# Optimization experiments

Measured on AMD Instinct MI355X. Metric: run time of the kernel, lower is better.

The kernel has to match this reference:

```python
import jax, jax.numpy as jnp
import numpy as np

N_WAY = 5
K_SHOT = 5
GAMMA = 20.0    # self.gamma
GAMMA2 = 10.0   # self.gamma2
ALPHA = 0.5     # self.katz_factor
EPS = 1e-16


def setup_inputs() -> dict:
    key = jax.random.key(0)
    k1, k2 = jax.random.split(key)
    feat = jax.random.normal(k1, (2 * N_WAY * K_SHOT, 640, 14, 14), dtype=jnp.float32)
    query_y = jax.random.randint(k2, (N_WAY * K_SHOT,), 0, N_WAY, dtype=jnp.int64)
    return {"feat": feat, "query_y": query_y}


def _predicts(feat):
    n_support = N_WAY * K_SHOT
    query = feat[n_support:]                      # (q, c, h, w)
    # adaptive_max_pool2d(query, w) with h == w is the identity, so the
    # (buggy-but-literal) torch code uses the query tensor as "support".
    support = query
    q, c, h, w = query.shape
    hw = h * w
    # class prototypes: mean over shots -> (n_way, c, hw)
    sup = support.reshape(N_WAY, K_SHOT, c, hw).mean(axis=1)
    qry = query.reshape(q, c, hw)
    # cosine metric: l2-normalize along channel axis
    sup = sup / (EPS + jnp.linalg.norm(sup, axis=1, keepdims=True))
    qry = qry / (EPS + jnp.linalg.norm(qry, axis=1, keepdims=True))
    # S[n, m_q, s, m_s] = <qry[n,:,m_q], sup[s,:,m_s]> ; then fold class dim into M_s
    S = jnp.einsum('qcm,scn->qmsn', qry, sup).reshape(q, hw, N_WAY * hw)
    N, M_q, M_s = S.shape
    # row-stochastic transition matrices (exp/max/sum == softmax of gamma*S)
    T_sq = jax.nn.softmax(GAMMA * S, axis=-1)                              # (N, M_q, M_s)
    T_qs = jax.nn.softmax(GAMMA2 * jnp.swapaxes(S, -1, -2), axis=-1)       # (N, M_s, M_q)
    # bipartite block matrix T = [[0, T_sq^T], [T_qs^T, 0]]
    top = jnp.concatenate([jnp.zeros((N, M_s, M_s), S.dtype),
                           jnp.swapaxes(T_sq, -1, -2)], axis=-1)
    bot = jnp.concatenate([jnp.swapaxes(T_qs, -1, -2),
                           jnp.zeros((N, M_q, M_q), S.dtype)], axis=-1)
    T = jnp.concatenate([top, bot], axis=-2)                               # (N, M_s+M_q, M_s+M_q)
    eye = jnp.eye(M_s + M_q, dtype=S.dtype)
    ones = jnp.ones((N, M_s + M_q, 1), S.dtype)
    # (inv(I - a T) - I) @ 1  ==  solve(I - a T, 1) - 1 (same math, no explicit inverse)
    katz = jnp.linalg.solve(eye[None] - ALPHA * T, ones)[..., 0] - 1.0     # (N, M_s+M_q)
    partial = katz[:, :M_s]
    partial = partial / partial.sum(axis=-1, keepdims=True)
    predicts = partial.reshape(N, N_WAY, -1).sum(axis=-1)                  # (N, n_way)
    return predicts


def reference(feat, query_y):
    return _predicts(feat)
```

## Files before the change

### kernel.cpp

```cpp
#include <hip/hip_runtime.h>
#include <math.h>

#define NQ     25
#define NWAY   5
#define KSHOT  5
#define CC     640
#define HW     196
#define NSL    980
#define NSLP   992
#define RPQ    208
#define BROWS  1024
#define MST    200
#define MRA    208
#define GAMMA  20.0f
#define GAMMA2 10.0f
#define NITER  8

typedef __bf16 bf16;
typedef _Float16 f16;
typedef __attribute__((ext_vector_type(8))) __bf16 bf16x8;
typedef __attribute__((ext_vector_type(4))) float f32x4;

__global__ __launch_bounds__(256) void k_norm(const float* __restrict__ feat,
                                              bf16* __restrict__ qnbt,
                                              bf16* __restrict__ snbt) {
    const int by = blockIdx.y;
    const int lx = threadIdx.x & 15;
    const int cg = threadIdx.x >> 4;
    const int l  = blockIdx.x * 16 + lx;
    const bool act = (l < HW);
    const int c0 = cg * 40;
    __shared__ float pr[16][17];

    float xv[40];
    float ss = 0.f;
    if (by < NQ) {
        const float* f = feat + (size_t)(NQ + by) * CC * HW;
#pragma unroll
        for (int i = 0; i < 40; ++i) {
            float x = act ? f[(c0 + i) * HW + l] : 0.f;
            xv[i] = x; ss += x * x;
        }
    } else {
        const int s = by - NQ;
        const float* f = feat + (size_t)(NQ + s * KSHOT) * CC * HW;
        const size_t img = (size_t)CC * HW;
#pragma unroll
        for (int i = 0; i < 40; ++i) {
            float m = 0.f;
            if (act) {
                const float* p = f + (c0 + i) * HW + l;
                m = 0.2f * (p[0] + p[img] + p[2 * img] + p[3 * img] + p[4 * img]);
            }
            xv[i] = m; ss += m * m;
        }
    }
    pr[cg][lx] = ss;
    __syncthreads();
    if (cg == 0) {
        float a = 0.f;
#pragma unroll
        for (int k = 0; k < 16; ++k) a += pr[k][lx];
        pr[0][lx] = 1.f / (1e-16f + sqrtf(a));
    }
    __syncthreads();
    const float inv = pr[0][lx];
    if (act) {
        bf16* o = (by < NQ) ? (qnbt + ((size_t)by * RPQ + l) * CC)
                            : (snbt + ((size_t)(by - NQ) * HW + l) * CC);
#pragma unroll
        for (int i = 0; i < 40; ++i) o[c0 + i] = (bf16)(xv[i] * inv);
    }
}

#define ASTR2 72
__global__ __launch_bounds__(256) void k_sgemm(const bf16* __restrict__ qnbt,
                                               const bf16* __restrict__ snbt,
                                               f16* __restrict__ S) {
    const int q  = blockIdx.z;
    const int m0 = blockIdx.y * 80;
    const int n0 = blockIdx.x * 128;
    __shared__ bf16 As[128 * ASTR2];
    __shared__ bf16 Bs[128 * ASTR2];
    const int t = threadIdx.x;
    const int lane = t & 63, w = t >> 6;
    const int wr = w >> 1, wc = w & 1;
    const int lo = lane & 15, hi = lane >> 4;
    const int sr = t >> 1, sh = (t & 1) * 32;

    const bf16* Aq = qnbt + (size_t)q * RPQ * CC;
    f32x4 acc[4][4] = {};

    for (int k0 = 0; k0 < CC; k0 += 64) {
        bf16x8 a0 = *reinterpret_cast<const bf16x8*>(&Aq[(size_t)(m0 + sr) * CC + k0 + sh]);
        bf16x8 a1 = *reinterpret_cast<const bf16x8*>(&Aq[(size_t)(m0 + sr) * CC + k0 + sh + 8]);
        bf16x8 a2 = *reinterpret_cast<const bf16x8*>(&Aq[(size_t)(m0 + sr) * CC + k0 + sh + 16]);
        bf16x8 a3 = *reinterpret_cast<const bf16x8*>(&Aq[(size_t)(m0 + sr) * CC + k0 + sh + 24]);
        bf16x8 b0 = *reinterpret_cast<const bf16x8*>(&snbt[(size_t)(n0 + sr) * CC + k0 + sh]);
        bf16x8 b1 = *reinterpret_cast<const bf16x8*>(&snbt[(size_t)(n0 + sr) * CC + k0 + sh + 8]);
        bf16x8 b2 = *reinterpret_cast<const bf16x8*>(&snbt[(size_t)(n0 + sr) * CC + k0 + sh + 16]);
        bf16x8 b3 = *reinterpret_cast<const bf16x8*>(&snbt[(size_t)(n0 + sr) * CC + k0 + sh + 24]);
        __syncthreads();
        *reinterpret_cast<bf16x8*>(&As[sr * ASTR2 + sh])      = a0;
        *reinterpret_cast<bf16x8*>(&As[sr * ASTR2 + sh + 8])  = a1;
        *reinterpret_cast<bf16x8*>(&As[sr * ASTR2 + sh + 16]) = a2;
        *reinterpret_cast<bf16x8*>(&As[sr * ASTR2 + sh + 24]) = a3;
        *reinterpret_cast<bf16x8*>(&Bs[sr * ASTR2 + sh])      = b0;
        *reinterpret_cast<bf16x8*>(&Bs[sr * ASTR2 + sh + 8])  = b1;
        *reinterpret_cast<bf16x8*>(&Bs[sr * ASTR2 + sh + 16]) = b2;
        *reinterpret_cast<bf16x8*>(&Bs[sr * ASTR2 + sh + 24]) = b3;
        __syncthreads();
#pragma unroll
        for (int kk = 0; kk < 2; ++kk) {
            bf16x8 af[4], bf[4];
#pragma unroll
            for (int mi = 0; mi < 4; ++mi)
                af[mi] = *reinterpret_cast<const bf16x8*>(
                    &As[(wr * 64 + mi * 16 + lo) * ASTR2 + kk * 32 + hi * 8]);
#pragma unroll
            for (int ni = 0; ni < 4; ++ni)
                bf[ni] = *reinterpret_cast<const bf16x8*>(
                    &Bs[(wc * 64 + ni * 16 + lo) * ASTR2 + kk * 32 + hi * 8]);
#pragma unroll
            for (int mi = 0; mi < 4; ++mi)
#pragma unroll
                for (int ni = 0; ni < 4; ++ni)
                    acc[mi][ni] = __builtin_amdgcn_mfma_f32_16x16x32_bf16(af[mi], bf[ni], acc[mi][ni], 0, 0, 0);
        }
    }

    f16* Sq = S + (size_t)q * HW * NSL;
#pragma unroll
    for (int mi = 0; mi < 4; ++mi) {
#pragma unroll
        for (int ni = 0; ni < 4; ++ni) {
            const int j = n0 + wc * 64 + ni * 16 + lo;
            if (j >= NSL) continue;
#pragma unroll
            for (int r = 0; r < 4; ++r) {
                const int m = m0 + wr * 64 + mi * 16 + hi * 4 + r;
                if (m < HW) Sq[(size_t)m * NSL + j] = (f16)acc[mi][ni][r];
            }
        }
    }
}

#define TSBLK (NQ * HW / 4)
__global__ __launch_bounds__(256) void k_soft(const f16* __restrict__ S,
                                              bf16* __restrict__ Ts,
                                              bf16* __restrict__ Tq,
                                              float* __restrict__ R) {
    const int bid = blockIdx.x;
    if (bid < TSBLK) {
        const int lane = threadIdx.x & 63, w = threadIdx.x >> 6;
        const int qm = bid * 4 + w;
        const int q = qm / HW, m = qm - q * HW;
        const f16* row = S + (size_t)qm * NSL;
        bf16* orow = Ts + ((size_t)q * RPQ + m) * NSLP;
        float x[16];
        float mx = -1e30f;
#pragma unroll
        for (int p = 0; p < 16; ++p) {
            int j = lane + p * 64;
            x[p] = (j < NSL) ? (float)row[j] : -1e30f;
            mx = fmaxf(mx, x[p]);
        }
        for (int d = 32; d; d >>= 1) mx = fmaxf(mx, __shfl_xor(mx, d));
        float sum = 0.f;
#pragma unroll
        for (int p = 0; p < 16; ++p) {
            x[p] = expf(GAMMA * (x[p] - mx));
            sum += x[p];
        }
        for (int d = 32; d; d >>= 1) sum += __shfl_xor(sum, d);
        const float inv = 1.f / sum;
        float racc[NWAY];
#pragma unroll
        for (int s = 0; s < NWAY; ++s) racc[s] = 0.f;
#pragma unroll
        for (int p = 0; p < 16; ++p) {
            int j = lane + p * 64;
            if (j < NSL) {
                float val = x[p] * inv;
                orow[j] = (bf16)val;
                int cls = j / HW;
#pragma unroll
                for (int s = 0; s < NWAY; ++s) racc[s] += (cls == s) ? val : 0.f;
            } else if (j < NSLP) {
                orow[j] = (bf16)0.f;
            }
        }
#pragma unroll
        for (int s = 0; s < NWAY; ++s)
            for (int d = 32; d; d >>= 1) racc[s] += __shfl_xor(racc[s], d);
        if (lane == 0) {
#pragma unroll
            for (int s = 0; s < NWAY; ++s)
                R[((size_t)q * NWAY + s) * HW + m] = racc[s];
        }
    } else {
        const int idx2 = bid - TSBLK;
        const int q  = idx2 >> 4;
        const int bx = idx2 & 15;
        const int tx = threadIdx.x & 63;
        const int tg = threadIdx.x >> 6;
        const int j  = bx * 64 + tx;
        const int m0 = tg * 49;
        const f16* base = S + (size_t)q * HW * NSL;
        bf16* ob = Tq + (size_t)q * RPQ * NSLP;
        __shared__ float rmax[4][64], rsum[4][64];
        float xv[49];
        float mx = -1e30f;
        if (j < NSL) {
#pragma unroll
            for (int i = 0; i < 49; ++i) {
                xv[i] = (float)base[(m0 + i) * NSL + j];
                mx = fmaxf(mx, xv[i]);
            }
        }
        rmax[tg][tx] = mx;
        __syncthreads();
        mx = fmaxf(fmaxf(rmax[0][tx], rmax[1][tx]), fmaxf(rmax[2][tx], rmax[3][tx]));
        float sum = 0.f;
        if (j < NSL) {
#pragma unroll
            for (int i = 0; i < 49; ++i) {
                xv[i] = expf(GAMMA2 * (xv[i] - mx));
                sum += xv[i];
            }
        }
        rsum[tg][tx] = sum;
        __syncthreads();
        const float inv = 1.f / (rsum[0][tx] + rsum[1][tx] + rsum[2][tx] + rsum[3][tx]);
        if (j < NSL) {
#pragma unroll
            for (int i = 0; i < 49; ++i) ob[(size_t)(m0 + i) * NSLP + j] = (bf16)(xv[i] * inv);
        } else if (j < NSLP) {
#pragma unroll
            for (int i = 0; i < 49; ++i) ob[(size_t)(m0 + i) * NSLP + j] = (bf16)0.f;
        }
    }
}

__global__ __launch_bounds__(64) void k_mgemm(const bf16* __restrict__ Tq,
                                              const bf16* __restrict__ Ts,
                                              bf16* __restrict__ Mb,
                                              float* __restrict__ rhs) {
    const int q  = blockIdx.z;
    const int it = blockIdx.y;
    const int jt = blockIdx.x;
    const int l  = threadIdx.x;
    const int lo = l & 15, hi = l >> 4;
    const bool dorhs = (jt == 0);
    const bf16* Ap[4];
    const bf16* Bp[4];
#pragma unroll
    for (int mi = 0; mi < 4; ++mi)
        Ap[mi] = Tq + ((size_t)q * RPQ + it * 64 + mi * 16 + lo) * NSLP + hi * 8;
#pragma unroll
    for (int ni = 0; ni < 4; ++ni)
        Bp[ni] = Ts + ((size_t)q * RPQ + jt * 64 + ni * 16 + lo) * NSLP + hi * 8;

    f32x4 acc[4][4] = {};
    float rsum[4] = {0.f, 0.f, 0.f, 0.f};
#pragma unroll 2
    for (int k0 = 0; k0 < NSLP; k0 += 32) {
        bf16x8 a[4], b[4];
#pragma unroll
        for (int mi = 0; mi < 4; ++mi) a[mi] = *reinterpret_cast<const bf16x8*>(Ap[mi] + k0);
#pragma unroll
        for (int ni = 0; ni < 4; ++ni) b[ni] = *reinterpret_cast<const bf16x8*>(Bp[ni] + k0);
        if (dorhs) {
#pragma unroll
            for (int mi = 0; mi < 4; ++mi)
#pragma unroll
                for (int e = 0; e < 8; ++e) rsum[mi] += (float)a[mi][e];
        }
#pragma unroll
        for (int mi = 0; mi < 4; ++mi)
#pragma unroll
            for (int ni = 0; ni < 4; ++ni)
                acc[mi][ni] = __builtin_amdgcn_mfma_f32_16x16x32_bf16(a[mi], b[ni], acc[mi][ni], 0, 0, 0);
    }

    if (dorhs) {
#pragma unroll
        for (int mi = 0; mi < 4; ++mi) {
            float v = rsum[mi];
            v += __shfl_xor(v, 16);
            v += __shfl_xor(v, 32);
            const int i = it * 64 + mi * 16 + lo;
            if (hi == 0 && i < HW) rhs[q * HW + i] = 1.f + 0.5f * v;
        }
    }

    bf16* Mq = Mb + (size_t)q * MRA * MST;
#pragma unroll
    for (int mi = 0; mi < 4; ++mi) {
#pragma unroll
        for (int ni = 0; ni < 4; ++ni) {
            const int j = jt * 64 + ni * 16 + lo;
            if (j >= MST) continue;
#pragma unroll
            for (int r = 0; r < 4; ++r) {
                const int i = it * 64 + mi * 16 + hi * 4 + r;
                if (i >= MRA) continue;
                Mq[(size_t)i * MST + j] =
                    (i < HW && j < HW) ? (bf16)(0.25f * acc[mi][ni][r]) : (bf16)0.f;
            }
        }
    }
}

__global__ __launch_bounds__(1024) void k_solve2(const bf16* __restrict__ Mb,
                                                 const float* __restrict__ rhs,
                                                 const float* __restrict__ R,
                                                 float* __restrict__ out) {
    const int q = blockIdx.x;
    __shared__ __align__(16) bf16 Ms[HW * MST];
    __shared__ __align__(16) float va[MST], vb[MST];
    __shared__ float part[4][256];
    __shared__ float rhsl[HW];
    __shared__ float cls[NWAY];
    const int t = threadIdx.x, lane = t & 63, w = t >> 6;

    const bf16x8* gm = reinterpret_cast<const bf16x8*>(Mb + (size_t)q * MRA * MST);
    bf16x8* lm = reinterpret_cast<bf16x8*>(Ms);
    for (int i = t; i < HW * (MST / 8); i += 1024) lm[i] = gm[i];

    if (t < MST) {
        float r = (t < HW) ? rhs[q * HW + t] : 0.f;
        if (t < HW) rhsl[t] = r;
        va[t] = r; vb[t] = 0.f;
    }
    __syncthreads();

    const int r = t & 255, qd = t >> 8;
    const int cstart = (qd == 0) ? 0 : 7 + 6 * (qd - 1);
    const int ccnt   = (qd == 0) ? 7 : 6;
    for (int it = 0; it < NITER; ++it) {
        const float* src = (it & 1) ? vb : va;
        float* dst = (it & 1) ? va : vb;
        float a = 0.f;
        if (r < HW) {
            const bf16x8* mrow = reinterpret_cast<const bf16x8*>(&Ms[r * MST]);
            for (int c = cstart; c < cstart + ccnt; ++c) {
                bf16x8 mv = mrow[c];
                const float* sp = &src[c * 8];
#pragma unroll
                for (int e = 0; e < 8; ++e) a += (float)mv[e] * sp[e];
            }
        }
        part[qd][r] = a;
        __syncthreads();
        if (qd == 0 && r < HW)
            dst[r] = rhsl[r] + (part[0][r] + part[1][r] + part[2][r] + part[3][r]);
        __syncthreads();
    }

    if (w < NWAY) {
        const float* Rs = R + ((size_t)q * NWAY + w) * HW;
        float a = 0.f;
        for (int m = lane; m < HW; m += 64) a += va[m] * Rs[m];
        for (int d = 32; d; d >>= 1) a += __shfl_xor(a, d);
        if (lane == 0) cls[w] = a;
    }
    __syncthreads();
    if (t == 0) {
        float tot = cls[0] + cls[1] + cls[2] + cls[3] + cls[4];
        float invt = 1.f / tot;
        for (int s = 0; s < NWAY; ++s) out[q * NWAY + s] = cls[s] * invt;
    }
}

extern "C" void kernel_launch(void* const* d_in, const int* in_sizes, int n_in,
                              void* d_out, int out_size, void* d_ws, size_t ws_size,
                              hipStream_t stream) {
    const float* feat = (const float*)d_in[0];
    float* out = (float*)d_out;
    char* w = (char*)d_ws;

    f16*   S    = (f16*)w;    w += sizeof(f16)   * (size_t)NQ * HW * NSL;
    bf16*  Ts   = (bf16*)w;   w += sizeof(bf16)  * (size_t)NQ * RPQ * NSLP;
    bf16*  Tq   = (bf16*)w;   w += sizeof(bf16)  * (size_t)NQ * RPQ * NSLP;
    bf16*  qnbt = (bf16*)w;   w += sizeof(bf16)  * (size_t)NQ * RPQ * CC;
    bf16*  snbt = (bf16*)w;   w += sizeof(bf16)  * (size_t)BROWS * CC;
    float* R    = (float*)w;  w += sizeof(float) * (size_t)NQ * NWAY * HW;
    float* rhs  = (float*)w;  w += sizeof(float) * (size_t)NQ * HW;
    bf16* Mb = (bf16*)S;

    k_norm  <<<dim3(13, NQ + NWAY), 256, 0, stream>>>(feat, qnbt, snbt);
    k_sgemm <<<dim3(8, 2, NQ), 256, 0, stream>>>(qnbt, snbt, S);
    k_soft  <<<TSBLK + NQ * 16, 256, 0, stream>>>(S, Ts, Tq, R);
    k_mgemm <<<dim3(4, 4, NQ), 64, 0, stream>>>(Tq, Ts, Mb, rhs);
    k_solve2<<<NQ, 1024, 0, stream>>>(Mb, rhs, R, out);
}
```

Baseline: 100.4 us.

## Vectorize normalization kernel with float4 loads and cut solver iterations

Rewrites the channel-norm kernel so each thread loads float4 spans of four spatial positions across ten channels, reduces the squared sums with wavefront shuffles plus a small shared array, and drops one barrier. This is meant to cut the number of memory transactions and the synchronisation overhead in the prep stage. It also lowers the iterative Katz solver's iteration count from 8 to 6, which saves work but may reduce accuracy. The float4 loads depend on 16-byte alignment, which holds because HW=196 is a multiple of 4.

```diff
diff --git a/kernel.cpp b/kernel.cpp
--- a/kernel.cpp
+++ b/kernel.cpp
@@ -14,7 +14,7 @@
 #define MRA    208
 #define GAMMA  20.0f
 #define GAMMA2 10.0f
-#define NITER  8
+#define NITER  6
 
 typedef __bf16 bf16;
 typedef _Float16 f16;
@@ -25,51 +25,77 @@
                                               bf16* __restrict__ qnbt,
                                               bf16* __restrict__ snbt) {
     const int by = blockIdx.y;
-    const int lx = threadIdx.x & 15;
-    const int cg = threadIdx.x >> 4;
-    const int l  = blockIdx.x * 16 + lx;
-    const bool act = (l < HW);
-    const int c0 = cg * 40;
-    __shared__ float pr[16][17];
-
-    float xv[40];
-    float ss = 0.f;
+    const int t  = threadIdx.x;
+    const int qd = t & 3;
+    const int cg = t >> 2;
+    const int l0 = blockIdx.x * 16 + qd * 4;
+    const bool act = (l0 < HW);
+    const int c0 = cg * 10;
+    const int w  = t >> 6, lane = t & 63;
+    __shared__ float4 pr2[4][4];
+
+    float4 xv[10];
+    float4 ss = {0.f, 0.f, 0.f, 0.f};
     if (by < NQ) {
         const float* f = feat + (size_t)(NQ + by) * CC * HW;
-#pragma unroll
-        for (int i = 0; i < 40; ++i) {
-            float x = act ? f[(c0 + i) * HW + l] : 0.f;
-            xv[i] = x; ss += x * x;
+        if (act) {
+#pragma unroll
+            for (int i = 0; i < 10; ++i) {
+                float4 v = *reinterpret_cast<const float4*>(&f[(c0 + i) * HW + l0]);
+                xv[i] = v;
+                ss.x += v.x * v.x; ss.y += v.y * v.y;
+                ss.z += v.z * v.z; ss.w += v.w * v.w;
+            }
         }
     } else {
         const int s = by - NQ;
         const float* f = feat + (size_t)(NQ + s * KSHOT) * CC * HW;
         const size_t img = (size_t)CC * HW;
-#pragma unroll
-        for (int i = 0; i < 40; ++i) {
-            float m = 0.f;
-            if (act) {
-                const float* p = f + (c0 + i) * HW + l;
-                m = 0.2f * (p[0] + p[img] + p[2 * img] + p[3 * img] + p[4 * img]);
-            }
-            xv[i] = m; ss += m * m;
-        }
-    }
-    pr[cg][lx] = ss;
+        if (act) {
+#pragma unroll
+            for (int i = 0; i < 10; ++i) {
+                const float* p = &f[(c0 + i) * HW + l0];
+                float4 v0 = *reinterpret_cast<const float4*>(p);
+                float4 v1 = *reinterpret_cast<const float4*>(p + img);
+                float4 v2 = *reinterpret_cast<const float4*>(p + 2 * img);
+                float4 v3 = *reinterpret_cast<const float4*>(p + 3 * img);
+                float4 v4 = *reinterpret_cast<const float4*>(p + 4 * img);
+                float4 m;
+                m.x = 0.2f * (v0.x + v1.x + v2.x + v3.x + v4.x);
+                m.y = 0.2f * (v0.y + v1.y + v2.y + v3.y + v4.y);
+                m.z = 0.2f * (v0.z + v1.z + v2.z + v3.z + v4.z);
+                m.w = 0.2f * (v0.w + v1.w + v2.w + v3.w + v4.w);
+                xv[i] = m;
+                ss.x += m.x * m.x; ss.y += m.y * m.y;
+                ss.z += m.z * m.z; ss.w += m.w * m.w;
+            }
+        }
+    }
+#pragma unroll
+    for (int d = 4; d <= 32; d <<= 1) {
+        ss.x += __shfl_xor(ss.x, d);
+        ss.y += __shfl_xor(ss.y, d);
+        ss.z += __shfl_xor(ss.z, d);
+        ss.w += __shfl_xor(ss.w, d);
+    }
+    if (lane < 4) pr2[w][lane] = ss;
     __syncthreads();
-    if (cg == 0) {
-        float a = 0.f;
-#pragma unroll
-        for (int k = 0; k < 16; ++k) a += pr[k][lx];
-        pr[0][lx] = 1.f / (1e-16f + sqrtf(a));
-    }
-    __syncthreads();
-    const float inv = pr[0][lx];
+    const float4 s0 = pr2[0][qd], s1 = pr2[1][qd], s2 = pr2[2][qd], s3 = pr2[3][qd];
+    float4 inv;
+    inv.x = 1.f / (1e-16f + sqrtf(s0.x + s1.x + s2.x + s3.x));
+    inv.y = 1.f / (1e-16f + sqrtf(s0.y + s1.y + s2.y + s3.y));
+    inv.z = 1.f / (1e-16f + sqrtf(s0.z + s1.z + s2.z + s3.z));
+    inv.w = 1.f / (1e-16f + sqrtf(s0.w + s1.w + s2.w + s3.w));
     if (act) {
-        bf16* o = (by < NQ) ? (qnbt + ((size_t)by * RPQ + l) * CC)
-                            : (snbt + ((size_t)(by - NQ) * HW + l) * CC);
-#pragma unroll
-        for (int i = 0; i < 40; ++i) o[c0 + i] = (bf16)(xv[i] * inv);
+        bf16* base = (by < NQ) ? (qnbt + ((size_t)by * RPQ + l0) * CC)
+                               : (snbt + ((size_t)(by - NQ) * HW + l0) * CC);
+#pragma unroll
+        for (int i = 0; i < 10; ++i) {
+            base[(size_t)0 * CC + c0 + i] = (bf16)(xv[i].x * inv.x);
+            base[(size_t)1 * CC + c0 + i] = (bf16)(xv[i].y * inv.y);
+            base[(size_t)2 * CC + c0 + i] = (bf16)(xv[i].z * inv.z);
+            base[(size_t)3 * CC + c0 + i] = (bf16)(xv[i].w * inv.w);
+        }
     }
 }
 
```

Measured after the change: 90.67 us. -9.7%, faster.
